# Optimization experiments

Hardware: AMD Instinct MI355X
Metric: run time of the kernel (lower is better)

## Reference

```python
import jax, jax.numpy as jnp
import numpy as np

ATT_HEADS = 4
H_FEATS = 16
IN_FEATS = 64
N_NODES = 50000
N_EDGES = 1000000


def setup_inputs() -> dict:
    key = jax.random.key(0)
    ks = jax.random.split(key, 12)
    h = jax.random.normal(ks[0], (N_NODES, IN_FEATS), dtype=jnp.float32)
    src_idx = jax.random.randint(ks[1], (N_EDGES,), 0, N_NODES)
    dst_idx = jax.random.randint(ks[2], (N_EDGES,), 0, N_NODES)
    s = 1.0 / np.sqrt(IN_FEATS)
    # w_liner: Linear(in_feats, h_feats*att_heads)
    W_w = jax.random.uniform(ks[3], (IN_FEATS, H_FEATS * ATT_HEADS), jnp.float32, -s, s)
    b_w = jax.random.uniform(ks[4], (H_FEATS * ATT_HEADS,), jnp.float32, -s, s)
    # atten: Linear(2*h_feats, 1)
    sa = 1.0 / np.sqrt(2 * H_FEATS)
    W_a = jax.random.uniform(ks[5], (2 * H_FEATS, 1), jnp.float32, -sa, sa)
    b_a = jax.random.uniform(ks[6], (1,), jnp.float32, -sa, sa)
    # relation_aware: d_liner Linear(in_feats, in_feats), f_liner Linear(3*in_feats, 1)
    W_d = jax.random.uniform(ks[7], (IN_FEATS, IN_FEATS), jnp.float32, -s, s)
    b_d = jax.random.uniform(ks[8], (IN_FEATS,), jnp.float32, -s, s)
    sf = 1.0 / np.sqrt(3 * IN_FEATS)
    W_f = jax.random.uniform(ks[9], (3 * IN_FEATS, 1), jnp.float32, -sf, sf)
    b_f = jax.random.uniform(ks[10], (1,), jnp.float32, -sf, sf)
    return {"h": h, "src_idx": src_idx, "dst_idx": dst_idx,
            "W_w": W_w, "b_w": b_w, "W_a": W_a, "b_a": b_a,
            "W_d": W_d, "b_d": b_d, "W_f": W_f, "b_f": b_f}


def reference(h, src_idx, dst_idx, W_w, b_w, W_a, b_a, W_d, b_d, W_f, b_f):
    N = h.shape[0]
    # sign_edges: relation_aware score -> sign per edge
    s_feat = h[src_idx] @ W_d + b_d            # [E, F]
    d_feat = h[dst_idx] @ W_d + b_d            # [E, F]
    e_feat = jnp.concatenate([s_feat, d_feat, s_feat - d_feat], axis=-1)
    score = jnp.tanh(e_feat @ W_f + b_f)[:, 0]  # [E]
    sign = jnp.sign(score)
    # node transform
    hp = h @ W_w + b_w                          # [N, H*hf]
    # message: signed src features, per-head concat with dst, attention logit
    sf = (sign[:, None] * hp[src_idx]).reshape(-1, ATT_HEADS, H_FEATS)  # [E,H,hf]
    df = hp[dst_idx].reshape(-1, ATT_HEADS, H_FEATS)                    # [E,H,hf]
    z = jnp.concatenate([sf, df], axis=-1)                              # [E,H,2hf]
    alpha = jax.nn.leaky_relu(z @ W_a + b_a)                            # [E,H,1]
    # reduce: segment softmax over incoming edges of each dst node
    amax = jax.ops.segment_max(alpha, dst_idx, num_segments=N)          # [N,H,1]
    ex = jnp.exp(alpha - amax[dst_idx])
    esum = jax.ops.segment_sum(ex, dst_idx, num_segments=N)             # [N,H,1]
    w = ex / esum[dst_idx]                                              # [E,H,1]
    out = jax.ops.segment_sum(w * sf, dst_idx, num_segments=N)          # [N,H,hf]
    return out.reshape(N, ATT_HEADS * H_FEATS)
```

## Files before the change

### kernel.cpp

```cpp
#include <hip/hip_runtime.h>
#include <hip/hip_fp16.h>

constexpr int F  = 64;
constexpr int HEADS = 4;
constexpr int K_SLOT = 64;

__global__ __launch_bounds__(256) void node_kernel(
    const float* __restrict__ h,
    const float* __restrict__ W_w, const float* __restrict__ b_w,
    const float* __restrict__ W_a,
    const float* __restrict__ W_d, const float* __restrict__ b_d,
    const float* __restrict__ W_f,
    float* __restrict__ tfeat, __half* __restrict__ hp,
    float* __restrict__ u_arr, float* __restrict__ v_arr,
    float* __restrict__ a_src, float* __restrict__ a_dst,
    unsigned* __restrict__ cnt, unsigned* __restrict__ of_cnt, int N, int nb)
{
    __shared__ float sWT[F * F];
    __shared__ float sb[F];
    __shared__ double swfA[F], swfB[F];
    __shared__ float sWa[32];

    int tid = threadIdx.x;
    bool isW = blockIdx.x >= nb;
    const float* Wsrc = isW ? W_w : W_d;
    for (int i = tid; i < F * F; i += 256) {
        int k = i >> 6, j = i & 63;
        sWT[j * F + k] = Wsrc[i];
    }
    if (tid < F) sb[tid] = isW ? b_w[tid] : b_d[tid];
    if (!isW && tid < F) {
        swfA[tid] = (double)W_f[tid] + (double)W_f[2 * F + tid];
        swfB[tid] = (double)W_f[F + tid] - (double)W_f[2 * F + tid];
    }
    if (isW && tid < 32) sWa[tid] = W_a[tid];
    if (blockIdx.x == 0 && tid == 0) *of_cnt = 0;
    __syncthreads();

    int blk = isW ? (blockIdx.x - nb) : blockIdx.x;
    int n = blk * 256 + tid;
    if (n >= N) return;

    if (!isW) cnt[n] = 0;

    float4 hv[16];
    const float4* h4 = reinterpret_cast<const float4*>(h + (size_t)n * F);
#pragma unroll
    for (int i = 0; i < 16; i++) hv[i] = h4[i];

    if (!isW) {
        double u = 0.0, v = 0.0;
        float4 tq;
        float4* trow = reinterpret_cast<float4*>(tfeat + (size_t)n * F);
#pragma unroll 4
        for (int j = 0; j < F; j++) {
            const float4* row = reinterpret_cast<const float4*>(&sWT[j * F]);
            float t = 0.f;
#pragma unroll
            for (int kk = 0; kk < 16; kk++) {
                float4 w = row[kk];
                float4 x = hv[kk];
                t = fmaf(x.x, w.x, t);
                t = fmaf(x.y, w.y, t);
                t = fmaf(x.z, w.z, t);
                t = fmaf(x.w, w.w, t);
            }
            t = t + sb[j];
            u = fma((double)t, swfA[j], u);
            v = fma((double)t, swfB[j], v);
            if ((j & 3) == 0) tq.x = t;
            else if ((j & 3) == 1) tq.y = t;
            else if ((j & 3) == 2) tq.z = t;
            else { tq.w = t; trow[j >> 2] = tq; }
        }
        u_arr[n] = (float)u;
        v_arr[n] = (float)v;
    } else {
        __half2* prow = reinterpret_cast<__half2*>(hp + (size_t)n * F);
#pragma unroll
        for (int qh = 0; qh < 4; qh++) {
            float asq = 0.f, adq = 0.f;
            float pprev = 0.f;
#pragma unroll 4
            for (int jj = 0; jj < 16; jj++) {
                int j = qh * 16 + jj;
                const float4* row = reinterpret_cast<const float4*>(&sWT[j * F]);
                float p = 0.f;
#pragma unroll
                for (int kk = 0; kk < 16; kk++) {
                    float4 w = row[kk];
                    float4 x = hv[kk];
                    p = fmaf(x.x, w.x, p);
                    p = fmaf(x.y, w.y, p);
                    p = fmaf(x.z, w.z, p);
                    p = fmaf(x.w, w.w, p);
                }
                p = p + sb[j];
                asq = fmaf(p, sWa[jj], asq);
                adq = fmaf(p, sWa[16 + jj], adq);
                if ((jj & 1) == 0) pprev = p;
                else prow[j >> 1] = __floats2half2_rn(pprev, p);
            }
            a_src[n * HEADS + qh] = asq;
            a_dst[n * HEADS + qh] = adq;
        }
    }
}

__device__ __noinline__ float tier2_sign(
    const float* __restrict__ tfeat, const float* __restrict__ sWf,
    int s, int d, float bf)
{
    const float4* ts = reinterpret_cast<const float4*>(tfeat + (size_t)s * F);
    const float4* td = reinterpret_cast<const float4*>(tfeat + (size_t)d * F);
    float sv[F];
#pragma unroll
    for (int i = 0; i < 16; i++) {
        float4 a = ts[i];
        sv[4 * i + 0] = a.x; sv[4 * i + 1] = a.y;
        sv[4 * i + 2] = a.z; sv[4 * i + 3] = a.w;
    }
    float acc = 0.f;
#pragma unroll
    for (int j = 0; j < F; j++) acc = fmaf(sv[j], sWf[j], acc);
#pragma unroll
    for (int i = 0; i < 16; i++) {
        float4 a = td[i];
        acc = fmaf(a.x, sWf[F + 4 * i + 0], acc);
        acc = fmaf(a.y, sWf[F + 4 * i + 1], acc);
        acc = fmaf(a.z, sWf[F + 4 * i + 2], acc);
        acc = fmaf(a.w, sWf[F + 4 * i + 3], acc);
    }
#pragma unroll
    for (int i = 0; i < 16; i++) {
        float4 a = td[i];
        acc = fmaf(sv[4 * i + 0] - a.x, sWf[2 * F + 4 * i + 0], acc);
        acc = fmaf(sv[4 * i + 1] - a.y, sWf[2 * F + 4 * i + 1], acc);
        acc = fmaf(sv[4 * i + 2] - a.z, sWf[2 * F + 4 * i + 2], acc);
        acc = fmaf(sv[4 * i + 3] - a.w, sWf[2 * F + 4 * i + 3], acc);
    }
    float sp = acc + bf;
    return (sp > 0.f) ? 1.f : (sp < 0.f ? -1.f : 0.f);
}

__global__ __launch_bounds__(256) void count_scatter_kernel(
    const int* __restrict__ src_idx, const int* __restrict__ dst_idx,
    const float* __restrict__ u_arr, const float* __restrict__ v_arr,
    const float* __restrict__ tfeat, const float* __restrict__ W_f,
    const float* __restrict__ b_f,
    unsigned* __restrict__ cnt, unsigned* __restrict__ slot,
    unsigned* __restrict__ of_list, unsigned* __restrict__ of_cnt, int E)
{
    __shared__ float sWf[3 * F];
    int tid = threadIdx.x;
    if (tid < 3 * F) sWf[tid] = W_f[tid];
    __syncthreads();

    float bf = b_f[0];
    int e0 = blockIdx.x * 512 + tid;
    int e1 = e0 + 256;
    bool ok0 = e0 < E, ok1 = e1 < E;

    int s0 = 0, d0 = 0, s1 = 0, d1 = 0;
    if (ok0) { s0 = src_idx[e0]; d0 = dst_idx[e0]; }
    if (ok1) { s1 = src_idx[e1]; d1 = dst_idx[e1]; }

    float us0 = ok0 ? u_arr[s0] : 0.f, vd0 = ok0 ? v_arr[d0] : 0.f;
    float us1 = ok1 ? u_arr[s1] : 0.f, vd1 = ok1 ? v_arr[d1] : 0.f;
    unsigned p0 = ok0 ? atomicAdd(&cnt[d0], 1u) : 0u;
    unsigned p1 = ok1 ? atomicAdd(&cnt[d1], 1u) : 0u;

    float m0 = us0 + vd0 + bf;
    float m1 = us1 + vd1 + bf;

    float sg0 = (fabsf(m0) >= 1e-4f) ? ((m0 > 0.f) ? 1.f : -1.f)
                                     : (ok0 ? tier2_sign(tfeat, sWf, s0, d0, bf) : 0.f);
    float sg1 = (fabsf(m1) >= 1e-4f) ? ((m1 > 0.f) ? 1.f : -1.f)
                                     : (ok1 ? tier2_sign(tfeat, sWf, s1, d1, bf) : 0.f);

    if (ok0) {
        unsigned c0 = (sg0 > 0.f) ? 0u : (sg0 < 0.f ? 1u : 2u);
        unsigned val = (unsigned)s0 | (c0 << 30);
        if (p0 < (unsigned)K_SLOT) slot[(size_t)d0 * K_SLOT + p0] = val;
        else {
            unsigned oi = atomicAdd(of_cnt, 1u);
            of_list[2 * oi] = (unsigned)d0;
            of_list[2 * oi + 1] = val;
        }
    }
    if (ok1) {
        unsigned c1 = (sg1 > 0.f) ? 0u : (sg1 < 0.f ? 1u : 2u);
        unsigned val = (unsigned)s1 | (c1 << 30);
        if (p1 < (unsigned)K_SLOT) slot[(size_t)d1 * K_SLOT + p1] = val;
        else {
            unsigned oi = atomicAdd(of_cnt, 1u);
            of_list[2 * oi] = (unsigned)d1;
            of_list[2 * oi + 1] = val;
        }
    }
}

__global__ __launch_bounds__(256) void dst_gather_kernel(
    const unsigned* __restrict__ cnt,
    const unsigned* __restrict__ slot,
    const unsigned* __restrict__ of_list, const unsigned* __restrict__ of_cnt,
    const float* __restrict__ a_src, const float* __restrict__ a_dst,
    const float* __restrict__ b_a,
    const __half* __restrict__ hp,
    float* __restrict__ out, int N)
{
    __shared__ float sw[4][K_SLOT * 4];
    __shared__ unsigned ssrc[4][K_SLOT];

    int tid = threadIdx.x;
    int wslot = tid >> 6;
    int lane = tid & 63;
    int q = lane >> 4;
    int d = (blockIdx.x * 256 + tid) >> 6;
    bool valid = d < N;

    unsigned deg = 0;
    float ba = b_a[0];
    float4 ad4 = make_float4(0.f, 0.f, 0.f, 0.f);
    if (valid) {
        deg = cnt[d];
        ad4 = *reinterpret_cast<const float4*>(a_dst + (size_t)d * HEADS);
    }
    float adq = (q == 0) ? ad4.x : (q == 1) ? ad4.y : (q == 2) ? ad4.z : ad4.w;
    unsigned mdeg = min(deg, (unsigned)K_SLOT);

    float4 p = make_float4(0.f, 0.f, 0.f, 0.f);
    if (valid && lane < (int)mdeg) {
        unsigned sp = slot[(size_t)d * K_SLOT + lane];
        unsigned s = sp & 0x3FFFFFFFu;
        unsigned c = sp >> 30;
        float sgn = (c == 0u) ? 1.f : (c == 1u ? -1.f : 0.f);
        float4 as4 = *reinterpret_cast<const float4*>(a_src + (size_t)s * HEADS);
        float ap0 = fmaf(sgn, as4.x, ad4.x) + ba;
        float ap1 = fmaf(sgn, as4.y, ad4.y) + ba;
        float ap2 = fmaf(sgn, as4.z, ad4.z) + ba;
        float ap3 = fmaf(sgn, as4.w, ad4.w) + ba;
        float e0 = expf(ap0 > 0.f ? ap0 : 0.01f * ap0);
        float e1 = expf(ap1 > 0.f ? ap1 : 0.01f * ap1);
        float e2 = expf(ap2 > 0.f ? ap2 : 0.01f * ap2);
        float e3 = expf(ap3 > 0.f ? ap3 : 0.01f * ap3);
        p = make_float4(e0, e1, e2, e3);
        *reinterpret_cast<float4*>(&sw[wslot][lane * 4]) =
            make_float4(sgn * e0, sgn * e1, sgn * e2, sgn * e3);
        ssrc[wslot][lane] = s;
    }
    if (valid && deg > (unsigned)K_SLOT) {
        unsigned on = *of_cnt;
        for (unsigned i = lane; i < on; i += 64) {
            if (of_list[2 * i] == (unsigned)d) {
                unsigned sp = of_list[2 * i + 1];
                unsigned s = sp & 0x3FFFFFFFu;
                unsigned c = sp >> 30;
                float sgn = (c == 0u) ? 1.f : (c == 1u ? -1.f : 0.f);
                float4 as4 = *reinterpret_cast<const float4*>(a_src + (size_t)s * HEADS);
                float ap0 = fmaf(sgn, as4.x, ad4.x) + ba;
                float ap1 = fmaf(sgn, as4.y, ad4.y) + ba;
                float ap2 = fmaf(sgn, as4.z, ad4.z) + ba;
                float ap3 = fmaf(sgn, as4.w, ad4.w) + ba;
                p.x += expf(ap0 > 0.f ? ap0 : 0.01f * ap0);
                p.y += expf(ap1 > 0.f ? ap1 : 0.01f * ap1);
                p.z += expf(ap2 > 0.f ? ap2 : 0.01f * ap2);
                p.w += expf(ap3 > 0.f ? ap3 : 0.01f * ap3);
            }
        }
    }
    __syncthreads();

#pragma unroll
    for (int off = 32; off >= 1; off >>= 1) {
        p.x += __shfl_xor(p.x, off);
        p.y += __shfl_xor(p.y, off);
        p.z += __shfl_xor(p.z, off);
        p.w += __shfl_xor(p.w, off);
    }
    if (!valid) return;

    float esq = (q == 0) ? p.x : (q == 1) ? p.y : (q == 2) ? p.z : p.w;
    float rinv = (deg > 0) ? (1.0f / esq) : 0.f;

    const float* swb = &sw[wslot][0];
    const unsigned* ssb = &ssrc[wslot][0];

    float a0 = 0.f, a1 = 0.f, a2 = 0.f, a3 = 0.f;
    unsigned t0 = 0;
    for (; t0 + 8 <= mdeg; t0 += 8) {
        float w0 = swb[(t0 + 0) * 4 + q], w1 = swb[(t0 + 1) * 4 + q];
        float w2 = swb[(t0 + 2) * 4 + q], w3 = swb[(t0 + 3) * 4 + q];
        float w4 = swb[(t0 + 4) * 4 + q], w5 = swb[(t0 + 5) * 4 + q];
        float w6 = swb[(t0 + 6) * 4 + q], w7 = swb[(t0 + 7) * 4 + q];
        unsigned s0 = ssb[t0 + 0], s1 = ssb[t0 + 1];
        unsigned s2 = ssb[t0 + 2], s3 = ssb[t0 + 3];
        unsigned s4 = ssb[t0 + 4], s5 = ssb[t0 + 5];
        unsigned s6 = ssb[t0 + 6], s7 = ssb[t0 + 7];
        float h0 = __half2float(hp[((size_t)s0 << 6) | (unsigned)lane]);
        float h1 = __half2float(hp[((size_t)s1 << 6) | (unsigned)lane]);
        float h2 = __half2float(hp[((size_t)s2 << 6) | (unsigned)lane]);
        float h3 = __half2float(hp[((size_t)s3 << 6) | (unsigned)lane]);
        float h4 = __half2float(hp[((size_t)s4 << 6) | (unsigned)lane]);
        float h5 = __half2float(hp[((size_t)s5 << 6) | (unsigned)lane]);
        float h6 = __half2float(hp[((size_t)s6 << 6) | (unsigned)lane]);
        float h7 = __half2float(hp[((size_t)s7 << 6) | (unsigned)lane]);
        a0 = fmaf(w0, h0, a0); a1 = fmaf(w1, h1, a1);
        a2 = fmaf(w2, h2, a2); a3 = fmaf(w3, h3, a3);
        a0 = fmaf(w4, h4, a0); a1 = fmaf(w5, h5, a1);
        a2 = fmaf(w6, h6, a2); a3 = fmaf(w7, h7, a3);
    }
    for (; t0 < mdeg; t0++) {
        float w = swb[t0 * 4 + q];
        unsigned s = ssb[t0];
        a0 = fmaf(w, __half2float(hp[((size_t)s << 6) | (unsigned)lane]), a0);
    }
    if (deg > (unsigned)K_SLOT) {
        unsigned on = *of_cnt;
        for (unsigned i = 0; i < on; i++) {
            if (of_list[2 * i] == (unsigned)d) {
                unsigned sp = of_list[2 * i + 1];
                unsigned s = sp & 0x3FFFFFFFu;
                unsigned c = sp >> 30;
                float g = (c == 0u) ? 1.f : (c == 1u ? -1.f : 0.f);
                float asv = a_src[s * HEADS + q];
                float ap = fmaf(g, asv, adq) + ba;
                float ev = expf(ap > 0.f ? ap : 0.01f * ap);
                a0 = fmaf(ev * g, __half2float(hp[((size_t)s << 6) | (unsigned)lane]), a0);
            }
        }
    }
    out[((size_t)d << 6) | (unsigned)lane] = ((a0 + a1) + (a2 + a3)) * rinv;
}

extern "C" void kernel_launch(void* const* d_in, const int* in_sizes, int n_in,
                              void* d_out, int out_size, void* d_ws, size_t ws_size,
                              hipStream_t stream)
{
    const float* h       = (const float*)d_in[0];
    const int*   src_idx = (const int*)d_in[1];
    const int*   dst_idx = (const int*)d_in[2];
    const float* W_w     = (const float*)d_in[3];
    const float* b_w     = (const float*)d_in[4];
    const float* W_a     = (const float*)d_in[5];
    const float* b_a     = (const float*)d_in[6];
    const float* W_d     = (const float*)d_in[7];
    const float* b_d     = (const float*)d_in[8];
    const float* W_f     = (const float*)d_in[9];
    const float* b_f     = (const float*)d_in[10];

    int N = in_sizes[0] / F;
    int E = in_sizes[1];
    int nb = (N + 255) / 256;

    char* ws = (char*)d_ws;
    float*    tfeat  = (float*)ws;     ws += (size_t)N * F * 4;
    __half*   hp     = (__half*)ws;    ws += (size_t)N * F * 2;
    float*    u_arr  = (float*)ws;     ws += (size_t)N * 4;
    float*    v_arr  = (float*)ws;     ws += (size_t)N * 4;
    float*    a_src  = (float*)ws;     ws += (size_t)N * HEADS * 4;
    float*    a_dst  = (float*)ws;     ws += (size_t)N * HEADS * 4;
    unsigned* cnt    = (unsigned*)ws;  ws += (size_t)N * 4;
    unsigned* of_cnt = (unsigned*)ws;  ws += 64;
    unsigned* slot   = (unsigned*)ws;  ws += (size_t)N * K_SLOT * 4;
    unsigned* of_list= (unsigned*)ws;  ws += (size_t)E * 8;

    float* out = (float*)d_out;

    node_kernel<<<2 * nb, 256, 0, stream>>>(
        h, W_w, b_w, W_a, W_d, b_d, W_f, tfeat, hp, u_arr, v_arr, a_src, a_dst,
        cnt, of_cnt, N, nb);

    count_scatter_kernel<<<(E + 511) / 512, 256, 0, stream>>>(
        src_idx, dst_idx, u_arr, v_arr, tfeat, W_f, b_f,
        cnt, slot, of_list, of_cnt, E);

    dst_gather_kernel<<<(N * 64 + 255) / 256, 256, 0, stream>>>(
        cnt, slot, of_list, of_cnt, a_src, a_dst, b_a, hp, out, N);
}
```

Measured before the change: 138.4 us.

## Move W_w node transform into scatter kernel and pad per-node counters

Splits the node kernel so the W_d pass runs first and the W_w/attention projection runs as extra blocks inside the edge count/scatter kernel. This lets the W_w work overlap with the atomic-heavy edge scatter and makes the first kernel smaller. Per-node counters are also padded to 16 words (64 bytes) each, so atomics on nearby destinations no longer share a cache line. The padding multiplies the counter footprint and scatters the counter reads in the gather kernel across more memory.

```diff
diff --git a/kernel.cpp b/kernel.cpp
--- a/kernel.cpp
+++ b/kernel.cpp
@@ -4,78 +4,144 @@
 constexpr int F  = 64;
 constexpr int HEADS = 4;
 constexpr int K_SLOT = 64;
-
-__global__ __launch_bounds__(256) void node_kernel(
+constexpr int CPAD = 16;
+
+__global__ __launch_bounds__(256) void node_wd_kernel(
     const float* __restrict__ h,
-    const float* __restrict__ W_w, const float* __restrict__ b_w,
-    const float* __restrict__ W_a,
     const float* __restrict__ W_d, const float* __restrict__ b_d,
     const float* __restrict__ W_f,
-    float* __restrict__ tfeat, __half* __restrict__ hp,
+    float* __restrict__ tfeat,
     float* __restrict__ u_arr, float* __restrict__ v_arr,
-    float* __restrict__ a_src, float* __restrict__ a_dst,
-    unsigned* __restrict__ cnt, unsigned* __restrict__ of_cnt, int N, int nb)
+    unsigned* __restrict__ cnt, unsigned* __restrict__ of_cnt, int N)
 {
     __shared__ float sWT[F * F];
     __shared__ float sb[F];
     __shared__ double swfA[F], swfB[F];
-    __shared__ float sWa[32];
 
     int tid = threadIdx.x;
-    bool isW = blockIdx.x >= nb;
-    const float* Wsrc = isW ? W_w : W_d;
     for (int i = tid; i < F * F; i += 256) {
         int k = i >> 6, j = i & 63;
-        sWT[j * F + k] = Wsrc[i];
-    }
-    if (tid < F) sb[tid] = isW ? b_w[tid] : b_d[tid];
-    if (!isW && tid < F) {
+        sWT[j * F + k] = W_d[i];
+    }
+    if (tid < F) {
+        sb[tid] = b_d[tid];
         swfA[tid] = (double)W_f[tid] + (double)W_f[2 * F + tid];
         swfB[tid] = (double)W_f[F + tid] - (double)W_f[2 * F + tid];
     }
-    if (isW && tid < 32) sWa[tid] = W_a[tid];
     if (blockIdx.x == 0 && tid == 0) *of_cnt = 0;
     __syncthreads();
 
-    int blk = isW ? (blockIdx.x - nb) : blockIdx.x;
-    int n = blk * 256 + tid;
+    int n = blockIdx.x * 256 + tid;
     if (n >= N) return;
 
-    if (!isW) cnt[n] = 0;
+    cnt[(size_t)n * CPAD] = 0;
 
     float4 hv[16];
     const float4* h4 = reinterpret_cast<const float4*>(h + (size_t)n * F);
 #pragma unroll
     for (int i = 0; i < 16; i++) hv[i] = h4[i];
 
-    if (!isW) {
-        double u = 0.0, v = 0.0;
-        float4 tq;
-        float4* trow = reinterpret_cast<float4*>(tfeat + (size_t)n * F);
+    double u = 0.0, v = 0.0;
+    float4 tq;
+    float4* trow = reinterpret_cast<float4*>(tfeat + (size_t)n * F);
 #pragma unroll 4
-        for (int j = 0; j < F; j++) {
-            const float4* row = reinterpret_cast<const float4*>(&sWT[j * F]);
-            float t = 0.f;
-#pragma unroll
-            for (int kk = 0; kk < 16; kk++) {
-                float4 w = row[kk];
-                float4 x = hv[kk];
-                t = fmaf(x.x, w.x, t);
-                t = fmaf(x.y, w.y, t);
-                t = fmaf(x.z, w.z, t);
-                t = fmaf(x.w, w.w, t);
-            }
-            t = t + sb[j];
-            u = fma((double)t, swfA[j], u);
-            v = fma((double)t, swfB[j], v);
-            if ((j & 3) == 0) tq.x = t;
-            else if ((j & 3) == 1) tq.y = t;
-            else if ((j & 3) == 2) tq.z = t;
-            else { tq.w = t; trow[j >> 2] = tq; }
-        }
-        u_arr[n] = (float)u;
-        v_arr[n] = (float)v;
-    } else {
+    for (int j = 0; j < F; j++) {
+        const float4* row = reinterpret_cast<const float4*>(&sWT[j * F]);
+        float t = 0.f;
+#pragma unroll
+        for (int kk = 0; kk < 16; kk++) {
+            float4 w = row[kk];
+            float4 x = hv[kk];
+            t = fmaf(x.x, w.x, t);
+            t = fmaf(x.y, w.y, t);
+            t = fmaf(x.z, w.z, t);
+            t = fmaf(x.w, w.w, t);
+        }
+        t = t + sb[j];
+        u = fma((double)t, swfA[j], u);
+        v = fma((double)t, swfB[j], v);
+        if ((j & 3) == 0) tq.x = t;
+        else if ((j & 3) == 1) tq.y = t;
+        else if ((j & 3) == 2) tq.z = t;
+        else { tq.w = t; trow[j >> 2] = tq; }
+    }
+    u_arr[n] = (float)u;
+    v_arr[n] = (float)v;
+}
+
+__device__ __noinline__ float tier2_sign(
+    const float* __restrict__ tfeat, const float* __restrict__ sWf,
+    int s, int d, float bf)
+{
+    const float4* ts = reinterpret_cast<const float4*>(tfeat + (size_t)s * F);
+    const float4* td = reinterpret_cast<const float4*>(tfeat + (size_t)d * F);
+    float sv[F];
+#pragma unroll
+    for (int i = 0; i < 16; i++) {
+        float4 a = ts[i];
+        sv[4 * i + 0] = a.x; sv[4 * i + 1] = a.y;
+        sv[4 * i + 2] = a.z; sv[4 * i + 3] = a.w;
+    }
+    float acc = 0.f;
+#pragma unroll
+    for (int j = 0; j < F; j++) acc = fmaf(sv[j], sWf[j], acc);
+#pragma unroll
+    for (int i = 0; i < 16; i++) {
+        float4 a = td[i];
+        acc = fmaf(a.x, sWf[F + 4 * i + 0], acc);
+        acc = fmaf(a.y, sWf[F + 4 * i + 1], acc);
+        acc = fmaf(a.z, sWf[F + 4 * i + 2], acc);
+        acc = fmaf(a.w, sWf[F + 4 * i + 3], acc);
+    }
+#pragma unroll
+    for (int i = 0; i < 16; i++) {
+        float4 a = td[i];
+        acc = fmaf(sv[4 * i + 0] - a.x, sWf[2 * F + 4 * i + 0], acc);
+        acc = fmaf(sv[4 * i + 1] - a.y, sWf[2 * F + 4 * i + 1], acc);
+        acc = fmaf(sv[4 * i + 2] - a.z, sWf[2 * F + 4 * i + 2], acc);
+        acc = fmaf(sv[4 * i + 3] - a.w, sWf[2 * F + 4 * i + 3], acc);
+    }
+    float sp = acc + bf;
+    return (sp > 0.f) ? 1.f : (sp < 0.f ? -1.f : 0.f);
+}
+
+__global__ __launch_bounds__(256) void ww_count_scatter_kernel(
+    const float* __restrict__ h,
+    const float* __restrict__ W_w, const float* __restrict__ b_w,
+    const float* __restrict__ W_a,
+    __half* __restrict__ hp,
+    float* __restrict__ a_src, float* __restrict__ a_dst,
+    const int* __restrict__ src_idx, const int* __restrict__ dst_idx,
+    const float* __restrict__ u_arr, const float* __restrict__ v_arr,
+    const float* __restrict__ tfeat, const float* __restrict__ W_f,
+    const float* __restrict__ b_f,
+    unsigned* __restrict__ cnt, unsigned* __restrict__ slot,
+    unsigned* __restrict__ of_list, unsigned* __restrict__ of_cnt,
+    int N, int E, int nbw)
+{
+    __shared__ float sWT[F * F];
+    __shared__ float sb[F];
+    __shared__ float sWa[32];
+
+    int tid = threadIdx.x;
+
+    if (blockIdx.x < nbw) {
+        for (int i = tid; i < F * F; i += 256) {
+            int k = i >> 6, j = i & 63;
+            sWT[j * F + k] = W_w[i];
+        }
+        if (tid < F) sb[tid] = b_w[tid];
+        if (tid < 32) sWa[tid] = W_a[tid];
+        __syncthreads();
+
+        int n = blockIdx.x * 256 + tid;
+        if (n >= N) return;
+
+        float4 hv[16];
+        const float4* h4 = reinterpret_cast<const float4*>(h + (size_t)n * F);
+#pragma unroll
+        for (int i = 0; i < 16; i++) hv[i] = h4[i];
+
         __half2* prow = reinterpret_cast<__half2*>(hp + (size_t)n * F);
 #pragma unroll
         for (int qh = 0; qh < 4; qh++) {
@@ -104,60 +170,16 @@
             a_src[n * HEADS + qh] = asq;
             a_dst[n * HEADS + qh] = adq;
         }
-    }
-}
-
-__device__ __noinline__ float tier2_sign(
-    const float* __restrict__ tfeat, const float* __restrict__ sWf,
-    int s, int d, float bf)
-{
-    const float4* ts = reinterpret_cast<const float4*>(tfeat + (size_t)s * F);
-    const float4* td = reinterpret_cast<const float4*>(tfeat + (size_t)d * F);
-    float sv[F];
-#pragma unroll
-    for (int i = 0; i < 16; i++) {
-        float4 a = ts[i];
-        sv[4 * i + 0] = a.x; sv[4 * i + 1] = a.y;
-        sv[4 * i + 2] = a.z; sv[4 * i + 3] = a.w;
-    }
-    float acc = 0.f;
-#pragma unroll
-    for (int j = 0; j < F; j++) acc = fmaf(sv[j], sWf[j], acc);
-#pragma unroll
-    for (int i = 0; i < 16; i++) {
-        float4 a = td[i];
-        acc = fmaf(a.x, sWf[F + 4 * i + 0], acc);
-        acc = fmaf(a.y, sWf[F + 4 * i + 1], acc);
-        acc = fmaf(a.z, sWf[F + 4 * i + 2], acc);
-        acc = fmaf(a.w, sWf[F + 4 * i + 3], acc);
-    }
-#pragma unroll
-    for (int i = 0; i < 16; i++) {
-        float4 a = td[i];
-        acc = fmaf(sv[4 * i + 0] - a.x, sWf[2 * F + 4 * i + 0], acc);
-        acc = fmaf(sv[4 * i + 1] - a.y, sWf[2 * F + 4 * i + 1], acc);
-        acc = fmaf(sv[4 * i + 2] - a.z, sWf[2 * F + 4 * i + 2], acc);
-        acc = fmaf(sv[4 * i + 3] - a.w, sWf[2 * F + 4 * i + 3], acc);
-    }
-    float sp = acc + bf;
-    return (sp > 0.f) ? 1.f : (sp < 0.f ? -1.f : 0.f);
-}
-
-__global__ __launch_bounds__(256) void count_scatter_kernel(
-    const int* __restrict__ src_idx, const int* __restrict__ dst_idx,
-    const float* __restrict__ u_arr, const float* __restrict__ v_arr,
-    const float* __restrict__ tfeat, const float* __restrict__ W_f,
-    const float* __restrict__ b_f,
-    unsigned* __restrict__ cnt, unsigned* __restrict__ slot,
-    unsigned* __restrict__ of_list, unsigned* __restrict__ of_cnt, int E)
-{
-    __shared__ float sWf[3 * F];
-    int tid = threadIdx.x;
+        return;
+    }
+
+    float* sWf = sWT;
     if (tid < 3 * F) sWf[tid] = W_f[tid];
     __syncthreads();
 
     float bf = b_f[0];
-    int e0 = blockIdx.x * 512 + tid;
+    int eb = blockIdx.x - nbw;
+    int e0 = eb * 512 + tid;
     int e1 = e0 + 256;
     bool ok0 = e0 < E, ok1 = e1 < E;
 
@@ -167,8 +189,8 @@
 
     float us0 = ok0 ? u_arr[s0] : 0.f, vd0 = ok0 ? v_arr[d0] : 0.f;
     float us1 = ok1 ? u_arr[s1] : 0.f, vd1 = ok1 ? v_arr[d1] : 0.f;
-    unsigned p0 = ok0 ? atomicAdd(&cnt[d0], 1u) : 0u;
-    unsigned p1 = ok1 ? atomicAdd(&cnt[d1], 1u) : 0u;
+    unsigned p0 = ok0 ? atomicAdd(&cnt[(size_t)d0 * CPAD], 1u) : 0u;
+    unsigned p1 = ok1 ? atomicAdd(&cnt[(size_t)d1 * CPAD], 1u) : 0u;
 
     float m0 = us0 + vd0 + bf;
     float m1 = us1 + vd1 + bf;
@@ -223,7 +245,7 @@
     float ba = b_a[0];
     float4 ad4 = make_float4(0.f, 0.f, 0.f, 0.f);
     if (valid) {
-        deg = cnt[d];
+        deg = cnt[(size_t)d * CPAD];
         ad4 = *reinterpret_cast<const float4*>(a_dst + (size_t)d * HEADS);
     }
     float adq = (q == 0) ? ad4.x : (q == 1) ? ad4.y : (q == 2) ? ad4.z : ad4.w;
@@ -352,6 +374,7 @@
     int N = in_sizes[0] / F;
     int E = in_sizes[1];
     int nb = (N + 255) / 256;
+    int neb = (E + 511) / 512;
 
     char* ws = (char*)d_ws;
     float*    tfeat  = (float*)ws;     ws += (size_t)N * F * 4;
@@ -360,20 +383,20 @@
     float*    v_arr  = (float*)ws;     ws += (size_t)N * 4;
     float*    a_src  = (float*)ws;     ws += (size_t)N * HEADS * 4;
     float*    a_dst  = (float*)ws;     ws += (size_t)N * HEADS * 4;
-    unsigned* cnt    = (unsigned*)ws;  ws += (size_t)N * 4;
+    unsigned* cnt    = (unsigned*)ws;  ws += (size_t)N * CPAD * 4;
     unsigned* of_cnt = (unsigned*)ws;  ws += 64;
     unsigned* slot   = (unsigned*)ws;  ws += (size_t)N * K_SLOT * 4;
     unsigned* of_list= (unsigned*)ws;  ws += (size_t)E * 8;
 
     float* out = (float*)d_out;
 
-    node_kernel<<<2 * nb, 256, 0, stream>>>(
-        h, W_w, b_w, W_a, W_d, b_d, W_f, tfeat, hp, u_arr, v_arr, a_src, a_dst,
-        cnt, of_cnt, N, nb);
-
-    count_scatter_kernel<<<(E + 511) / 512, 256, 0, stream>>>(
+    node_wd_kernel<<<nb, 256, 0, stream>>>(
+        h, W_d, b_d, W_f, tfeat, u_arr, v_arr, cnt, of_cnt, N);
+
+    ww_count_scatter_kernel<<<nb + neb, 256, 0, stream>>>(
+        h, W_w, b_w, W_a, hp, a_src, a_dst,
         src_idx, dst_idx, u_arr, v_arr, tfeat, W_f, b_f,
-        cnt, slot, of_list, of_cnt, E);
+        cnt, slot, of_list, of_cnt, N, E, nb);
 
     dst_gather_kernel<<<(N * 64 + 255) / 256, 256, 0, stream>>>(
         cnt, slot, of_list, of_cnt, a_src, a_dst, b_a, hp, out, N);
```

After: 136.5 us. About the same (-1.4%).

## Fuse edge bucketing into node kernel and defer sign computation to gather

Applied to the files above, without the earlier changes.

The edge count/scatter pass now runs as extra blocks inside the node-transform kernel, so it overlaps with the per-node matmuls, and the counters are zeroed by a memset beforehand. Sign evaluation moves out of the scatter into the gather kernel, where each edge's sign is computed from u/v (with a tier-2 fallback) only when the edge is consumed. The overflow list is capped at E/8 entries. This drops one kernel launch and removes the dependency of scatter on node outputs. In exchange it adds a memset launch and extra u_arr/tfeat reads in the gather. Overflow edges beyond the cap would be silently dropped.

```diff
diff --git a/kernel.cpp b/kernel.cpp
--- a/kernel.cpp
+++ b/kernel.cpp
@@ -5,7 +5,37 @@
 constexpr int HEADS = 4;
 constexpr int K_SLOT = 64;
 
-__global__ __launch_bounds__(256) void node_kernel(
+__device__ __noinline__ float tier2_sign_stream(
+    const float* __restrict__ tfeat, const float* __restrict__ W_f,
+    int s, int d, float bf)
+{
+    const float4* ts = reinterpret_cast<const float4*>(tfeat + (size_t)s * F);
+    const float4* td = reinterpret_cast<const float4*>(tfeat + (size_t)d * F);
+    const float4* wf = reinterpret_cast<const float4*>(W_f);
+    float acc = 0.f;
+#pragma unroll
+    for (int i = 0; i < 16; i++) {
+        float4 a = ts[i], w = wf[i];
+        acc = fmaf(a.x, w.x, acc); acc = fmaf(a.y, w.y, acc);
+        acc = fmaf(a.z, w.z, acc); acc = fmaf(a.w, w.w, acc);
+    }
+#pragma unroll
+    for (int i = 0; i < 16; i++) {
+        float4 a = td[i], w = wf[16 + i];
+        acc = fmaf(a.x, w.x, acc); acc = fmaf(a.y, w.y, acc);
+        acc = fmaf(a.z, w.z, acc); acc = fmaf(a.w, w.w, acc);
+    }
+#pragma unroll
+    for (int i = 0; i < 16; i++) {
+        float4 a = ts[i], b = td[i], w = wf[32 + i];
+        acc = fmaf(a.x - b.x, w.x, acc); acc = fmaf(a.y - b.y, w.y, acc);
+        acc = fmaf(a.z - b.z, w.z, acc); acc = fmaf(a.w - b.w, w.w, acc);
+    }
+    float sp = acc + bf;
+    return (sp > 0.f) ? 1.f : (sp < 0.f ? -1.f : 0.f);
+}
+
+__global__ __launch_bounds__(256) void fused_kernel(
     const float* __restrict__ h,
     const float* __restrict__ W_w, const float* __restrict__ b_w,
     const float* __restrict__ W_a,
@@ -14,14 +44,48 @@
     float* __restrict__ tfeat, __half* __restrict__ hp,
     float* __restrict__ u_arr, float* __restrict__ v_arr,
     float* __restrict__ a_src, float* __restrict__ a_dst,
-    unsigned* __restrict__ cnt, unsigned* __restrict__ of_cnt, int N, int nb)
+    const int* __restrict__ src_idx, const int* __restrict__ dst_idx,
+    unsigned* __restrict__ cnt, unsigned* __restrict__ slot,
+    unsigned* __restrict__ of_list, unsigned* __restrict__ of_cnt,
+    int N, int E, int nb, unsigned of_cap)
 {
+    int tid = threadIdx.x;
+
+    if (blockIdx.x >= 2 * nb) {
+        int eb = blockIdx.x - 2 * nb;
+        int e0 = eb * 512 + tid;
+        int e1 = e0 + 256;
+        bool ok0 = e0 < E, ok1 = e1 < E;
+
+        int s0 = 0, d0 = 0, s1 = 0, d1 = 0;
+        if (ok0) { s0 = src_idx[e0]; d0 = dst_idx[e0]; }
+        if (ok1) { s1 = src_idx[e1]; d1 = dst_idx[e1]; }
+
+        unsigned p0 = ok0 ? atomicAdd(&cnt[d0], 1u) : 0u;
+        unsigned p1 = ok1 ? atomicAdd(&cnt[d1], 1u) : 0u;
+
+        if (ok0) {
+            if (p0 < (unsigned)K_SLOT) slot[(size_t)d0 * K_SLOT + p0] = (unsigned)s0;
+            else {
+                unsigned oi = atomicAdd(of_cnt, 1u);
+                if (oi < of_cap) { of_list[2 * oi] = (unsigned)d0; of_list[2 * oi + 1] = (unsigned)s0; }
+            }
+        }
+        if (ok1) {
+            if (p1 < (unsigned)K_SLOT) slot[(size_t)d1 * K_SLOT + p1] = (unsigned)s1;
+            else {
+                unsigned oi = atomicAdd(of_cnt, 1u);
+                if (oi < of_cap) { of_list[2 * oi] = (unsigned)d1; of_list[2 * oi + 1] = (unsigned)s1; }
+            }
+        }
+        return;
+    }
+
     __shared__ float sWT[F * F];
     __shared__ float sb[F];
     __shared__ double swfA[F], swfB[F];
     __shared__ float sWa[32];
 
-    int tid = threadIdx.x;
     bool isW = blockIdx.x >= nb;
     const float* Wsrc = isW ? W_w : W_d;
     for (int i = tid; i < F * F; i += 256) {
@@ -34,14 +98,11 @@
         swfB[tid] = (double)W_f[F + tid] - (double)W_f[2 * F + tid];
     }
     if (isW && tid < 32) sWa[tid] = W_a[tid];
-    if (blockIdx.x == 0 && tid == 0) *of_cnt = 0;
     __syncthreads();
 
     int blk = isW ? (blockIdx.x - nb) : blockIdx.x;
     int n = blk * 256 + tid;
     if (n >= N) return;
-
-    if (!isW) cnt[n] = 0;
 
     float4 hv[16];
     const float4* h4 = reinterpret_cast<const float4*>(h + (size_t)n * F);
@@ -107,107 +168,17 @@
     }
 }
 
-__device__ __noinline__ float tier2_sign(
-    const float* __restrict__ tfeat, const float* __restrict__ sWf,
-    int s, int d, float bf)
-{
-    const float4* ts = reinterpret_cast<const float4*>(tfeat + (size_t)s * F);
-    const float4* td = reinterpret_cast<const float4*>(tfeat + (size_t)d * F);
-    float sv[F];
-#pragma unroll
-    for (int i = 0; i < 16; i++) {
-        float4 a = ts[i];
-        sv[4 * i + 0] = a.x; sv[4 * i + 1] = a.y;
-        sv[4 * i + 2] = a.z; sv[4 * i + 3] = a.w;
-    }
-    float acc = 0.f;
-#pragma unroll
-    for (int j = 0; j < F; j++) acc = fmaf(sv[j], sWf[j], acc);
-#pragma unroll
-    for (int i = 0; i < 16; i++) {
-        float4 a = td[i];
-        acc = fmaf(a.x, sWf[F + 4 * i + 0], acc);
-        acc = fmaf(a.y, sWf[F + 4 * i + 1], acc);
-        acc = fmaf(a.z, sWf[F + 4 * i + 2], acc);
-        acc = fmaf(a.w, sWf[F + 4 * i + 3], acc);
-    }
-#pragma unroll
-    for (int i = 0; i < 16; i++) {
-        float4 a = td[i];
-        acc = fmaf(sv[4 * i + 0] - a.x, sWf[2 * F + 4 * i + 0], acc);
-        acc = fmaf(sv[4 * i + 1] - a.y, sWf[2 * F + 4 * i + 1], acc);
-        acc = fmaf(sv[4 * i + 2] - a.z, sWf[2 * F + 4 * i + 2], acc);
-        acc = fmaf(sv[4 * i + 3] - a.w, sWf[2 * F + 4 * i + 3], acc);
-    }
-    float sp = acc + bf;
-    return (sp > 0.f) ? 1.f : (sp < 0.f ? -1.f : 0.f);
-}
-
-__global__ __launch_bounds__(256) void count_scatter_kernel(
-    const int* __restrict__ src_idx, const int* __restrict__ dst_idx,
-    const float* __restrict__ u_arr, const float* __restrict__ v_arr,
-    const float* __restrict__ tfeat, const float* __restrict__ W_f,
-    const float* __restrict__ b_f,
-    unsigned* __restrict__ cnt, unsigned* __restrict__ slot,
-    unsigned* __restrict__ of_list, unsigned* __restrict__ of_cnt, int E)
-{
-    __shared__ float sWf[3 * F];
-    int tid = threadIdx.x;
-    if (tid < 3 * F) sWf[tid] = W_f[tid];
-    __syncthreads();
-
-    float bf = b_f[0];
-    int e0 = blockIdx.x * 512 + tid;
-    int e1 = e0 + 256;
-    bool ok0 = e0 < E, ok1 = e1 < E;
-
-    int s0 = 0, d0 = 0, s1 = 0, d1 = 0;
-    if (ok0) { s0 = src_idx[e0]; d0 = dst_idx[e0]; }
-    if (ok1) { s1 = src_idx[e1]; d1 = dst_idx[e1]; }
-
-    float us0 = ok0 ? u_arr[s0] : 0.f, vd0 = ok0 ? v_arr[d0] : 0.f;
-    float us1 = ok1 ? u_arr[s1] : 0.f, vd1 = ok1 ? v_arr[d1] : 0.f;
-    unsigned p0 = ok0 ? atomicAdd(&cnt[d0], 1u) : 0u;
-    unsigned p1 = ok1 ? atomicAdd(&cnt[d1], 1u) : 0u;
-
-    float m0 = us0 + vd0 + bf;
-    float m1 = us1 + vd1 + bf;
-
-    float sg0 = (fabsf(m0) >= 1e-4f) ? ((m0 > 0.f) ? 1.f : -1.f)
-                                     : (ok0 ? tier2_sign(tfeat, sWf, s0, d0, bf) : 0.f);
-    float sg1 = (fabsf(m1) >= 1e-4f) ? ((m1 > 0.f) ? 1.f : -1.f)
-                                     : (ok1 ? tier2_sign(tfeat, sWf, s1, d1, bf) : 0.f);
-
-    if (ok0) {
-        unsigned c0 = (sg0 > 0.f) ? 0u : (sg0 < 0.f ? 1u : 2u);
-        unsigned val = (unsigned)s0 | (c0 << 30);
-        if (p0 < (unsigned)K_SLOT) slot[(size_t)d0 * K_SLOT + p0] = val;
-        else {
-            unsigned oi = atomicAdd(of_cnt, 1u);
-            of_list[2 * oi] = (unsigned)d0;
-            of_list[2 * oi + 1] = val;
-        }
-    }
-    if (ok1) {
-        unsigned c1 = (sg1 > 0.f) ? 0u : (sg1 < 0.f ? 1u : 2u);
-        unsigned val = (unsigned)s1 | (c1 << 30);
-        if (p1 < (unsigned)K_SLOT) slot[(size_t)d1 * K_SLOT + p1] = val;
-        else {
-            unsigned oi = atomicAdd(of_cnt, 1u);
-            of_list[2 * oi] = (unsigned)d1;
-            of_list[2 * oi + 1] = val;
-        }
-    }
-}
-
 __global__ __launch_bounds__(256) void dst_gather_kernel(
     const unsigned* __restrict__ cnt,
     const unsigned* __restrict__ slot,
     const unsigned* __restrict__ of_list, const unsigned* __restrict__ of_cnt,
+    const float* __restrict__ u_arr, const float* __restrict__ v_arr,
+    const float* __restrict__ tfeat, const float* __restrict__ W_f,
+    const float* __restrict__ b_f,
     const float* __restrict__ a_src, const float* __restrict__ a_dst,
     const float* __restrict__ b_a,
     const __half* __restrict__ hp,
-    float* __restrict__ out, int N)
+    float* __restrict__ out, int N, unsigned of_cap)
 {
     __shared__ float sw[4][K_SLOT * 4];
     __shared__ unsigned ssrc[4][K_SLOT];
@@ -219,22 +190,26 @@
     int d = (blockIdx.x * 256 + tid) >> 6;
     bool valid = d < N;
 
+    float ba = b_a[0], bf = b_f[0];
+    float4 ad4 = make_float4(0.f, 0.f, 0.f, 0.f);
     unsigned deg = 0;
-    float ba = b_a[0];
-    float4 ad4 = make_float4(0.f, 0.f, 0.f, 0.f);
+    float vd = 0.f;
     if (valid) {
         deg = cnt[d];
         ad4 = *reinterpret_cast<const float4*>(a_dst + (size_t)d * HEADS);
+        vd = v_arr[d];
     }
     float adq = (q == 0) ? ad4.x : (q == 1) ? ad4.y : (q == 2) ? ad4.z : ad4.w;
     unsigned mdeg = min(deg, (unsigned)K_SLOT);
+    bool fast = valid && (deg <= (unsigned)K_SLOT);
 
     float4 p = make_float4(0.f, 0.f, 0.f, 0.f);
     if (valid && lane < (int)mdeg) {
-        unsigned sp = slot[(size_t)d * K_SLOT + lane];
-        unsigned s = sp & 0x3FFFFFFFu;
-        unsigned c = sp >> 30;
-        float sgn = (c == 0u) ? 1.f : (c == 1u ? -1.f : 0.f);
+        unsigned s = slot[(size_t)d * K_SLOT + lane];
+        float us = u_arr[s];
+        float m = us + vd + bf;
+        float sgn = (fabsf(m) >= 1e-4f) ? ((m > 0.f) ? 1.f : -1.f)
+                                        : tier2_sign_stream(tfeat, W_f, (int)s, d, bf);
         float4 as4 = *reinterpret_cast<const float4*>(a_src + (size_t)s * HEADS);
         float ap0 = fmaf(sgn, as4.x, ad4.x) + ba;
         float ap1 = fmaf(sgn, as4.y, ad4.y) + ba;
@@ -249,14 +224,15 @@
             make_float4(sgn * e0, sgn * e1, sgn * e2, sgn * e3);
         ssrc[wslot][lane] = s;
     }
-    if (valid && deg > (unsigned)K_SLOT) {
-        unsigned on = *of_cnt;
+    if (valid && !fast) {
+        unsigned on = min(*of_cnt, of_cap);
         for (unsigned i = lane; i < on; i += 64) {
             if (of_list[2 * i] == (unsigned)d) {
-                unsigned sp = of_list[2 * i + 1];
-                unsigned s = sp & 0x3FFFFFFFu;
-                unsigned c = sp >> 30;
-                float sgn = (c == 0u) ? 1.f : (c == 1u ? -1.f : 0.f);
+                unsigned s = of_list[2 * i + 1];
+                float us = u_arr[s];
+                float m = us + vd + bf;
+                float sgn = (fabsf(m) >= 1e-4f) ? ((m > 0.f) ? 1.f : -1.f)
+                                                : tier2_sign_stream(tfeat, W_f, (int)s, d, bf);
                 float4 as4 = *reinterpret_cast<const float4*>(a_src + (size_t)s * HEADS);
                 float ap0 = fmaf(sgn, as4.x, ad4.x) + ba;
                 float ap1 = fmaf(sgn, as4.y, ad4.y) + ba;
@@ -315,14 +291,15 @@
         unsigned s = ssb[t0];
         a0 = fmaf(w, __half2float(hp[((size_t)s << 6) | (unsigned)lane]), a0);
     }
-    if (deg > (unsigned)K_SLOT) {
-        unsigned on = *of_cnt;
+    if (!fast) {
+        unsigned on = min(*of_cnt, of_cap);
         for (unsigned i = 0; i < on; i++) {
             if (of_list[2 * i] == (unsigned)d) {
-                unsigned sp = of_list[2 * i + 1];
-                unsigned s = sp & 0x3FFFFFFFu;
-                unsigned c = sp >> 30;
-                float g = (c == 0u) ? 1.f : (c == 1u ? -1.f : 0.f);
+                unsigned s = of_list[2 * i + 1];
+                float us = u_arr[s];
+                float m = us + vd + bf;
+                float g = (fabsf(m) >= 1e-4f) ? ((m > 0.f) ? 1.f : -1.f)
+                                              : tier2_sign_stream(tfeat, W_f, (int)s, d, bf);
                 float asv = a_src[s * HEADS + q];
                 float ap = fmaf(g, asv, adq) + ba;
                 float ev = expf(ap > 0.f ? ap : 0.01f * ap);
@@ -352,6 +329,8 @@
     int N = in_sizes[0] / F;
     int E = in_sizes[1];
     int nb = (N + 255) / 256;
+    int neb = (E + 511) / 512;
+    unsigned of_cap = (unsigned)(E / 8);
 
     char* ws = (char*)d_ws;
     float*    tfeat  = (float*)ws;     ws += (size_t)N * F * 4;
@@ -363,18 +342,19 @@
     unsigned* cnt    = (unsigned*)ws;  ws += (size_t)N * 4;
     unsigned* of_cnt = (unsigned*)ws;  ws += 64;
     unsigned* slot   = (unsigned*)ws;  ws += (size_t)N * K_SLOT * 4;
-    unsigned* of_list= (unsigned*)ws;  ws += (size_t)E * 8;
+    unsigned* of_list= (unsigned*)ws;  ws += (size_t)of_cap * 8;
 
     float* out = (float*)d_out;
 
-    node_kernel<<<2 * nb, 256, 0, stream>>>(
-        h, W_w, b_w, W_a, W_d, b_d, W_f, tfeat, hp, u_arr, v_arr, a_src, a_dst,
-        cnt, of_cnt, N, nb);
-
-    count_scatter_kernel<<<(E + 511) / 512, 256, 0, stream>>>(
-        src_idx, dst_idx, u_arr, v_arr, tfeat, W_f, b_f,
-        cnt, slot, of_list, of_cnt, E);
+    hipMemsetAsync(cnt, 0, (size_t)N * 4 + 64, stream);
+
+    fused_kernel<<<2 * nb + neb, 256, 0, stream>>>(
+        h, W_w, b_w, W_a, W_d, b_d, W_f,
+        tfeat, hp, u_arr, v_arr, a_src, a_dst,
+        src_idx, dst_idx, cnt, slot, of_list, of_cnt,
+        N, E, nb, of_cap);
 
     dst_gather_kernel<<<(N * 64 + 255) / 256, 256, 0, stream>>>(
-        cnt, slot, of_list, of_cnt, a_src, a_dst, b_a, hp, out, N);
+        cnt, slot, of_list, of_cnt, u_arr, v_arr, tfeat, W_f, b_f,
+        a_src, a_dst, b_a, hp, out, N, of_cap);
 }
```

After: 189.8 us. +37.1%, slower.
